# Performance work log

Measured on AMD Instinct MI355X. Metric: run time of the kernel, lower is better.

Reference implementation:

```python
import jax, jax.numpy as jnp
import numpy as np

N_NODES = 100000
HIDDEN = 128
N_EDGES = 1600000


def setup_inputs() -> dict:
    key = jax.random.key(0)
    k_x, k_w, k_r, k_c = jax.random.split(key, 4)
    x = jax.random.normal(k_x, (4, N_NODES, HIDDEN), dtype=jnp.float32)
    W = jax.random.normal(k_w, (HIDDEN, HIDDEN), dtype=jnp.float32) * 0.05
    b = jnp.zeros((HIDDEN,), dtype=jnp.float32)
    # COO edge list of the block-diagonal adjacency (scipy.sparse.block_diag in original)
    rows = jax.random.randint(k_r, (N_EDGES,), 0, N_NODES, dtype=jnp.int64)
    cols = jax.random.randint(k_c, (N_EDGES,), 0, N_NODES, dtype=jnp.int64)
    return {"x": x, "W": W, "b": b, "rows": rows, "cols": cols}


def reference(x, W, b, rows, cols):
    n_nodes = x.shape[1]
    beta = x[3, :, 0]   # [N]
    gamma = x[3, :, 1]  # [N]
    # linear + sigmoid on S/I/R channels: [3, N, H]
    sir = jax.nn.sigmoid(jnp.einsum('snh,oh->sno', x[:3], W) + b)
    S, I = sir[0], sir[1]
    # AI[r] += I[c] for each edge (r, c) of block-diagonal adjacency
    AI = jax.ops.segment_sum(I[cols], rows, num_segments=n_nodes)
    dS = -beta[:, None] * AI * S
    dI = -dS - gamma[:, None] * I
    dR = gamma[:, None] * I
    return jnp.stack((dS, dI, dR, jnp.zeros_like(dS)))
```

## Files before the change

### kernel.cpp

```cpp
#include <hip/hip_runtime.h>
#include <math.h>

#define HD 128
#define BM 128

typedef short bf16x8 __attribute__((ext_vector_type(8)));
typedef float f32x4 __attribute__((ext_vector_type(4)));
typedef unsigned short u16;

static __device__ __forceinline__ u16 f2bf(float f) {
  unsigned int u = __float_as_uint(f);
  u += 0x7FFF + ((u >> 16) & 1);
  return (u16)(u >> 16);
}
static __device__ __forceinline__ float bf2f(u16 s) {
  return __uint_as_float(((unsigned int)s) << 16);
}

__global__ void __launch_bounds__(256) zero_kernel(float4* __restrict__ p, long n4) {
  long i = (long)blockIdx.x * blockDim.x + threadIdx.x;
  long stride = (long)gridDim.x * blockDim.x;
  float4 z = make_float4(0.f, 0.f, 0.f, 0.f);
  for (; i < n4; i += stride) p[i] = z;
}

__global__ void __launch_bounds__(256) hist_rows(const int* __restrict__ rows,
                                                 int* __restrict__ cnt, int n_edges) {
  int i = blockIdx.x * 256 + threadIdx.x;
  int stride = gridDim.x * 256;
  for (; i < n_edges; i += stride) atomicAdd(&cnt[rows[i]], 1);
}

#define SCAN_E 2048
__global__ void __launch_bounds__(256) scan_block(const int* __restrict__ cnt,
                                                  int* __restrict__ off,
                                                  int* __restrict__ bsum, int n) {
  __shared__ int tsum[256];
  int tid = threadIdx.x;
  int base = blockIdx.x * SCAN_E + tid * 8;
  int vals[8];
  int s = 0;
#pragma unroll
  for (int k = 0; k < 8; ++k) {
    int idx = base + k;
    vals[k] = (idx < n) ? cnt[idx] : 0;
    s += vals[k];
  }
  tsum[tid] = s;
  __syncthreads();
  for (int o = 1; o < 256; o <<= 1) {
    int add = (tid >= o) ? tsum[tid - o] : 0;
    __syncthreads();
    tsum[tid] += add;
    __syncthreads();
  }
  int tbase = tsum[tid] - s;
  int run = 0;
#pragma unroll
  for (int k = 0; k < 8; ++k) {
    int idx = base + k;
    if (idx < n) off[idx] = tbase + run;
    run += vals[k];
  }
  if (tid == 255) bsum[blockIdx.x] = tsum[255];
}

__global__ void __launch_bounds__(256) scan_add(int* __restrict__ off,
                                                const int* __restrict__ bsum,
                                                int nb, int n, int n_edges) {
  __shared__ int sAdd;
  if (threadIdx.x == 0) {
    int acc = 0;
    for (int i = 0; i < (int)blockIdx.x; ++i) acc += bsum[i];
    sAdd = acc;
  }
  __syncthreads();
  int add = sAdd;
  int base = blockIdx.x * SCAN_E + threadIdx.x * 8;
#pragma unroll
  for (int k = 0; k < 8; ++k) {
    int idx = base + k;
    if (idx < n) off[idx] += add;
  }
  if (blockIdx.x == 0 && threadIdx.x == 0) off[n] = n_edges;
}

__global__ void __launch_bounds__(512, 4) fill_gemm(
    const float* __restrict__ x, const float* __restrict__ W,
    const float* __restrict__ b, float* __restrict__ SI, int nrows,
    const int* __restrict__ rows, const int* __restrict__ cols,
    const int* __restrict__ off, int* __restrict__ cursor,
    int* __restrict__ ecol, int n_edges, int fblocks) {
  __shared__ u16 Wh[HD * HD];
  __shared__ u16 Wl[HD * HD];

  int tid = threadIdx.x;
  if (blockIdx.x < fblocks) {
    int i = blockIdx.x * 512 + tid;
    int stride = fblocks * 512;
    for (; i < n_edges; i += stride) {
      int r = rows[i];
      int p = atomicAdd(&cursor[r], 1);
      ecol[off[r] + p] = cols[i];
    }
    return;
  }

  for (int idx = tid; idx < HD * (HD / 8); idx += 512) {
    int r = idx >> 4;
    int c = idx & 15;
    const float4* src = (const float4*)(W + r * HD + c * 8);
    float4 a0 = src[0], a1 = src[1];
    float f[8] = {a0.x, a0.y, a0.z, a0.w, a1.x, a1.y, a1.z, a1.w};
    union { u16 s[8]; uint4 v; } Ph, Pl;
#pragma unroll
    for (int i = 0; i < 8; ++i) {
      u16 h = f2bf(f[i]);
      Ph.s[i] = h;
      Pl.s[i] = f2bf(f[i] - bf2f(h));
    }
    int dst = r * HD + ((c ^ (r & 15)) << 3);
    *(uint4*)&Wh[dst] = Ph.v;
    *(uint4*)&Wl[dst] = Pl.v;
  }
  __syncthreads();

  int w = tid >> 6;
  int l = tid & 63;
  int lr = l & 15;
  int lk = l >> 4;
  int rbase = (blockIdx.x - fblocks) * BM + w * 16;
  int arow = rbase + lr;
  bool rowok = arow < nrows;

  bf16x8 ah[4], al[4];
#pragma unroll
  for (int s = 0; s < 4; ++s) {
    float f[8] = {0.f, 0.f, 0.f, 0.f, 0.f, 0.f, 0.f, 0.f};
    if (rowok) {
      const float4* src = (const float4*)(x + (long)arow * HD + (s * 4 + lk) * 8);
      float4 a0 = src[0], a1 = src[1];
      f[0] = a0.x; f[1] = a0.y; f[2] = a0.z; f[3] = a0.w;
      f[4] = a1.x; f[5] = a1.y; f[6] = a1.z; f[7] = a1.w;
    }
    union { u16 s16[8]; bf16x8 v; } Ph, Pl;
#pragma unroll
    for (int i = 0; i < 8; ++i) {
      u16 h = f2bf(f[i]);
      Ph.s16[i] = h;
      Pl.s16[i] = f2bf(f[i] - bf2f(h));
    }
    ah[s] = Ph.v;
    al[s] = Pl.v;
  }

#pragma unroll
  for (int ct = 0; ct < 8; ++ct) {
    int col = ct * 16 + lr;
    f32x4 acc = {0.f, 0.f, 0.f, 0.f};
#pragma unroll
    for (int s = 0; s < 4; ++s) {
      int cb = ((s * 4 + lk) ^ lr) << 3;
      bf16x8 bh = *(const bf16x8*)&Wh[col * HD + cb];
      bf16x8 bl = *(const bf16x8*)&Wl[col * HD + cb];
      acc = __builtin_amdgcn_mfma_f32_16x16x32_bf16(ah[s], bh, acc, 0, 0, 0);
      acc = __builtin_amdgcn_mfma_f32_16x16x32_bf16(al[s], bh, acc, 0, 0, 0);
      acc = __builtin_amdgcn_mfma_f32_16x16x32_bf16(ah[s], bl, acc, 0, 0, 0);
    }
    float bb = b[col];
#pragma unroll
    for (int j = 0; j < 4; ++j) {
      int grow = rbase + lk * 4 + j;
      if (grow < nrows) {
        float v = acc[j] + bb;
        SI[(long)grow * HD + col] = 1.f / (1.f + __expf(-v));
      }
    }
  }
}

__global__ void __launch_bounds__(256) gather_finalize(const float* __restrict__ S,
                                                       const float* __restrict__ I,
                                                       const float* __restrict__ x3,
                                                       const int* __restrict__ off,
                                                       const int* __restrict__ ecol,
                                                       float* __restrict__ out,
                                                       int n_nodes) {
  int node = blockIdx.x * 4 + (threadIdx.x >> 6);
  if (node >= n_nodes) return;
  int lane = threadIdx.x & 63;

  int beg = off[node], end = off[node + 1];
  float2 acc = make_float2(0.f, 0.f);
  for (int j0 = beg; j0 < end; j0 += 64) {
    int myc = (j0 + lane < end) ? ecol[j0 + lane] : 0;
    int cnt = min(64, end - j0);
    int j = 0;
    for (; j + 3 < cnt; j += 4) {
      int c0 = __shfl(myc, j);
      int c1 = __shfl(myc, j + 1);
      int c2 = __shfl(myc, j + 2);
      int c3 = __shfl(myc, j + 3);
      float2 v0 = ((const float2*)(I + (long)c0 * HD))[lane];
      float2 v1 = ((const float2*)(I + (long)c1 * HD))[lane];
      float2 v2 = ((const float2*)(I + (long)c2 * HD))[lane];
      float2 v3 = ((const float2*)(I + (long)c3 * HD))[lane];
      acc.x += (v0.x + v1.x) + (v2.x + v3.x);
      acc.y += (v0.y + v1.y) + (v2.y + v3.y);
    }
    for (; j < cnt; ++j) {
      int c0 = __shfl(myc, j);
      float2 v0 = ((const float2*)(I + (long)c0 * HD))[lane];
      acc.x += v0.x;
      acc.y += v0.y;
    }
  }

  float beta  = x3[(long)node * HD + 0];
  float gamma = x3[(long)node * HD + 1];
  float2 s  = ((const float2*)(S + (long)node * HD))[lane];
  float2 ii = ((const float2*)(I + (long)node * HD))[lane];

  float2 dS, dI, dR;
  dS.x = -beta * acc.x * s.x;
  dS.y = -beta * acc.y * s.y;
  dI.x = -dS.x - gamma * ii.x;
  dI.y = -dS.y - gamma * ii.y;
  dR.x = gamma * ii.x;
  dR.y = gamma * ii.y;

  long p = (long)node * (HD / 2) + lane;
  long plane = (long)n_nodes * (HD / 2);
  float2* o = (float2*)out;
  o[p] = dS;
  o[plane + p] = dI;
  o[2 * plane + p] = dR;
  o[3 * plane + p] = make_float2(0.f, 0.f);
}

extern "C" void kernel_launch(void* const* d_in, const int* in_sizes, int n_in,
                              void* d_out, int out_size, void* d_ws, size_t ws_size,
                              hipStream_t stream) {
  const float* x = (const float*)d_in[0];
  const float* W = (const float*)d_in[1];
  const float* b = (const float*)d_in[2];
  const int* rows = (const int*)d_in[3];
  const int* cols = (const int*)d_in[4];
  float* out = (float*)d_out;

  int n_nodes = in_sizes[0] / (4 * HD);
  int n_edges = in_sizes[3];
  int nrows = 2 * n_nodes;

  float* S = (float*)d_ws;
  float* I = S + (long)n_nodes * HD;
  int* ib = (int*)(I + (long)n_nodes * HD);
  int npad = (n_nodes + 11) & ~3;
  int* counts  = ib;
  int* cursor  = counts + npad;
  int* offsets = cursor + npad;
  int* bsum    = offsets + npad;
  int* ecol    = bsum + 256;

  zero_kernel<<<(2 * npad / 4 + 255) / 256, 256, 0, stream>>>(
      (float4*)counts, 2 * npad / 4);

  hist_rows<<<512, 256, 0, stream>>>(rows, counts, n_edges);

  int nb = (n_nodes + SCAN_E - 1) / SCAN_E;
  scan_block<<<nb, 256, 0, stream>>>(counts, offsets, bsum, n_nodes);
  scan_add<<<nb, 256, 0, stream>>>(offsets, bsum, nb, n_nodes, n_edges);

  int gblocks = (nrows + BM - 1) / BM;
  int fblocks = 192;
  fill_gemm<<<fblocks + gblocks, 512, 0, stream>>>(
      x, W, b, S, nrows, rows, cols, offsets, cursor, ecol, n_edges, fblocks);

  int gfb = (n_nodes + 3) / 4;
  gather_finalize<<<gfb, 256, 0, stream>>>(S, I, x + 3 * (long)n_nodes * HD,
                                           offsets, ecol, out, n_nodes);
}
```

Before: 602.4 us.

## Fuse CSR build and GEMM into one persistent cooperative kernel with grid syncs

```diff
diff --git a/kernel.cpp b/kernel.cpp
--- a/kernel.cpp
+++ b/kernel.cpp
@@ -1,8 +1,13 @@
 #include <hip/hip_runtime.h>
+#include <hip/hip_cooperative_groups.h>
 #include <math.h>
+
+namespace cg = cooperative_groups;
 
 #define HD 128
 #define BM 128
+#define SCAN_E 2048
+#define HIST_B 64
 
 typedef short bf16x8 __attribute__((ext_vector_type(8)));
 typedef float f32x4 __attribute__((ext_vector_type(4)));
@@ -17,165 +22,157 @@
   return __uint_as_float(((unsigned int)s) << 16);
 }
 
-__global__ void __launch_bounds__(256) zero_kernel(float4* __restrict__ p, long n4) {
-  long i = (long)blockIdx.x * blockDim.x + threadIdx.x;
-  long stride = (long)gridDim.x * blockDim.x;
-  float4 z = make_float4(0.f, 0.f, 0.f, 0.f);
-  for (; i < n4; i += stride) p[i] = z;
-}
-
-__global__ void __launch_bounds__(256) hist_rows(const int* __restrict__ rows,
-                                                 int* __restrict__ cnt, int n_edges) {
-  int i = blockIdx.x * 256 + threadIdx.x;
-  int stride = gridDim.x * 256;
-  for (; i < n_edges; i += stride) atomicAdd(&cnt[rows[i]], 1);
-}
-
-#define SCAN_E 2048
-__global__ void __launch_bounds__(256) scan_block(const int* __restrict__ cnt,
-                                                  int* __restrict__ off,
-                                                  int* __restrict__ bsum, int n) {
-  __shared__ int tsum[256];
-  int tid = threadIdx.x;
-  int base = blockIdx.x * SCAN_E + tid * 8;
-  int vals[8];
-  int s = 0;
-#pragma unroll
-  for (int k = 0; k < 8; ++k) {
-    int idx = base + k;
-    vals[k] = (idx < n) ? cnt[idx] : 0;
-    s += vals[k];
-  }
-  tsum[tid] = s;
-  __syncthreads();
-  for (int o = 1; o < 256; o <<= 1) {
-    int add = (tid >= o) ? tsum[tid - o] : 0;
-    __syncthreads();
-    tsum[tid] += add;
-    __syncthreads();
-  }
-  int tbase = tsum[tid] - s;
-  int run = 0;
-#pragma unroll
-  for (int k = 0; k < 8; ++k) {
-    int idx = base + k;
-    if (idx < n) off[idx] = tbase + run;
-    run += vals[k];
-  }
-  if (tid == 255) bsum[blockIdx.x] = tsum[255];
-}
-
-__global__ void __launch_bounds__(256) scan_add(int* __restrict__ off,
-                                                const int* __restrict__ bsum,
-                                                int nb, int n, int n_edges) {
-  __shared__ int sAdd;
-  if (threadIdx.x == 0) {
-    int acc = 0;
-    for (int i = 0; i < (int)blockIdx.x; ++i) acc += bsum[i];
-    sAdd = acc;
-  }
-  __syncthreads();
-  int add = sAdd;
-  int base = blockIdx.x * SCAN_E + threadIdx.x * 8;
-#pragma unroll
-  for (int k = 0; k < 8; ++k) {
-    int idx = base + k;
-    if (idx < n) off[idx] += add;
-  }
-  if (blockIdx.x == 0 && threadIdx.x == 0) off[n] = n_edges;
-}
-
-__global__ void __launch_bounds__(512, 4) fill_gemm(
+__global__ void __launch_bounds__(512, 4) build_gemm_coop(
     const float* __restrict__ x, const float* __restrict__ W,
     const float* __restrict__ b, float* __restrict__ SI, int nrows,
     const int* __restrict__ rows, const int* __restrict__ cols,
-    const int* __restrict__ off, int* __restrict__ cursor,
-    int* __restrict__ ecol, int n_edges, int fblocks) {
+    int* __restrict__ counts, int* __restrict__ cursor,
+    int* __restrict__ offsets, int* __restrict__ bsum,
+    int* __restrict__ ecol, int n_edges, int n_nodes, int ntiles) {
+  cg::grid_group grid = cg::this_grid();
   __shared__ u16 Wh[HD * HD];
   __shared__ u16 Wl[HD * HD];
 
   int tid = threadIdx.x;
-  if (blockIdx.x < fblocks) {
-    int i = blockIdx.x * 512 + tid;
-    int stride = fblocks * 512;
-    for (; i < n_edges; i += stride) {
-      int r = rows[i];
-      int p = atomicAdd(&cursor[r], 1);
-      ecol[off[r] + p] = cols[i];
-    }
-    return;
-  }
-
-  for (int idx = tid; idx < HD * (HD / 8); idx += 512) {
-    int r = idx >> 4;
-    int c = idx & 15;
-    const float4* src = (const float4*)(W + r * HD + c * 8);
-    float4 a0 = src[0], a1 = src[1];
-    float f[8] = {a0.x, a0.y, a0.z, a0.w, a1.x, a1.y, a1.z, a1.w};
-    union { u16 s[8]; uint4 v; } Ph, Pl;
-#pragma unroll
-    for (int i = 0; i < 8; ++i) {
-      u16 h = f2bf(f[i]);
-      Ph.s[i] = h;
-      Pl.s[i] = f2bf(f[i] - bf2f(h));
-    }
-    int dst = r * HD + ((c ^ (r & 15)) << 3);
-    *(uint4*)&Wh[dst] = Ph.v;
-    *(uint4*)&Wl[dst] = Pl.v;
-  }
-  __syncthreads();
-
-  int w = tid >> 6;
-  int l = tid & 63;
-  int lr = l & 15;
-  int lk = l >> 4;
-  int rbase = (blockIdx.x - fblocks) * BM + w * 16;
-  int arow = rbase + lr;
-  bool rowok = arow < nrows;
-
-  bf16x8 ah[4], al[4];
-#pragma unroll
-  for (int s = 0; s < 4; ++s) {
-    float f[8] = {0.f, 0.f, 0.f, 0.f, 0.f, 0.f, 0.f, 0.f};
-    if (rowok) {
-      const float4* src = (const float4*)(x + (long)arow * HD + (s * 4 + lk) * 8);
+  int bid = blockIdx.x;
+  int B = gridDim.x;
+
+  for (int i = bid * 512 + tid; i < n_nodes; i += B * 512) counts[i] = 0;
+  grid.sync();
+
+  if (bid < HIST_B) {
+    for (int i = bid * 512 + tid; i < n_edges; i += HIST_B * 512)
+      atomicAdd(&counts[rows[i]], 1);
+  } else {
+    for (int idx = tid; idx < HD * (HD / 8); idx += 512) {
+      int r = idx >> 4;
+      int c = idx & 15;
+      const float4* src = (const float4*)(W + r * HD + c * 8);
       float4 a0 = src[0], a1 = src[1];
-      f[0] = a0.x; f[1] = a0.y; f[2] = a0.z; f[3] = a0.w;
-      f[4] = a1.x; f[5] = a1.y; f[6] = a1.z; f[7] = a1.w;
-    }
-    union { u16 s16[8]; bf16x8 v; } Ph, Pl;
-#pragma unroll
-    for (int i = 0; i < 8; ++i) {
-      u16 h = f2bf(f[i]);
-      Ph.s16[i] = h;
-      Pl.s16[i] = f2bf(f[i] - bf2f(h));
-    }
-    ah[s] = Ph.v;
-    al[s] = Pl.v;
-  }
-
-#pragma unroll
-  for (int ct = 0; ct < 8; ++ct) {
-    int col = ct * 16 + lr;
-    f32x4 acc = {0.f, 0.f, 0.f, 0.f};
-#pragma unroll
-    for (int s = 0; s < 4; ++s) {
-      int cb = ((s * 4 + lk) ^ lr) << 3;
-      bf16x8 bh = *(const bf16x8*)&Wh[col * HD + cb];
-      bf16x8 bl = *(const bf16x8*)&Wl[col * HD + cb];
-      acc = __builtin_amdgcn_mfma_f32_16x16x32_bf16(ah[s], bh, acc, 0, 0, 0);
-      acc = __builtin_amdgcn_mfma_f32_16x16x32_bf16(al[s], bh, acc, 0, 0, 0);
-      acc = __builtin_amdgcn_mfma_f32_16x16x32_bf16(ah[s], bl, acc, 0, 0, 0);
-    }
-    float bb = b[col];
-#pragma unroll
-    for (int j = 0; j < 4; ++j) {
-      int grow = rbase + lk * 4 + j;
-      if (grow < nrows) {
-        float v = acc[j] + bb;
-        SI[(long)grow * HD + col] = 1.f / (1.f + __expf(-v));
-      }
-    }
+      float f[8] = {a0.x, a0.y, a0.z, a0.w, a1.x, a1.y, a1.z, a1.w};
+      union { u16 s[8]; uint4 v; } Ph, Pl;
+#pragma unroll
+      for (int i = 0; i < 8; ++i) {
+        u16 h = f2bf(f[i]);
+        Ph.s[i] = h;
+        Pl.s[i] = f2bf(f[i] - bf2f(h));
+      }
+      int dst = r * HD + ((c ^ (r & 15)) << 3);
+      *(uint4*)&Wh[dst] = Ph.v;
+      *(uint4*)&Wl[dst] = Pl.v;
+    }
+    __syncthreads();
+
+    int w = tid >> 6;
+    int l = tid & 63;
+    int lr = l & 15;
+    int lk = l >> 4;
+    for (int tile = bid - HIST_B; tile < ntiles; tile += B - HIST_B) {
+      int rbase = tile * BM + w * 16;
+      int arow = rbase + lr;
+      bool rowok = arow < nrows;
+
+      bf16x8 ah[4], al[4];
+#pragma unroll
+      for (int s = 0; s < 4; ++s) {
+        float f[8] = {0.f, 0.f, 0.f, 0.f, 0.f, 0.f, 0.f, 0.f};
+        if (rowok) {
+          const float4* src = (const float4*)(x + (long)arow * HD + (s * 4 + lk) * 8);
+          float4 a0 = src[0], a1 = src[1];
+          f[0] = a0.x; f[1] = a0.y; f[2] = a0.z; f[3] = a0.w;
+          f[4] = a1.x; f[5] = a1.y; f[6] = a1.z; f[7] = a1.w;
+        }
+        union { u16 s16[8]; bf16x8 v; } Ph, Pl;
+#pragma unroll
+        for (int i = 0; i < 8; ++i) {
+          u16 h = f2bf(f[i]);
+          Ph.s16[i] = h;
+          Pl.s16[i] = f2bf(f[i] - bf2f(h));
+        }
+        ah[s] = Ph.v;
+        al[s] = Pl.v;
+      }
+
+#pragma unroll
+      for (int ct = 0; ct < 8; ++ct) {
+        int col = ct * 16 + lr;
+        f32x4 acc = {0.f, 0.f, 0.f, 0.f};
+#pragma unroll
+        for (int s = 0; s < 4; ++s) {
+          int cb = ((s * 4 + lk) ^ lr) << 3;
+          bf16x8 bh = *(const bf16x8*)&Wh[col * HD + cb];
+          bf16x8 bl = *(const bf16x8*)&Wl[col * HD + cb];
+          acc = __builtin_amdgcn_mfma_f32_16x16x32_bf16(ah[s], bh, acc, 0, 0, 0);
+          acc = __builtin_amdgcn_mfma_f32_16x16x32_bf16(al[s], bh, acc, 0, 0, 0);
+          acc = __builtin_amdgcn_mfma_f32_16x16x32_bf16(ah[s], bl, acc, 0, 0, 0);
+        }
+        float bb = b[col];
+#pragma unroll
+        for (int j = 0; j < 4; ++j) {
+          int grow = rbase + lk * 4 + j;
+          if (grow < nrows) {
+            float v = acc[j] + bb;
+            SI[(long)grow * HD + col] = 1.f / (1.f + __expf(-v));
+          }
+        }
+      }
+    }
+  }
+  grid.sync();
+
+  int NB = (n_nodes + SCAN_E - 1) / SCAN_E;
+  int* tsum = (int*)Wh;
+  if (bid < NB) {
+    int base = bid * SCAN_E + tid * 4;
+    int vals[4];
+    int s = 0;
+#pragma unroll
+    for (int k = 0; k < 4; ++k) {
+      int idx = base + k;
+      vals[k] = (idx < n_nodes) ? counts[idx] : 0;
+      s += vals[k];
+    }
+    tsum[tid] = s;
+    __syncthreads();
+    for (int o = 1; o < 512; o <<= 1) {
+      int add = (tid >= o) ? tsum[tid - o] : 0;
+      __syncthreads();
+      tsum[tid] += add;
+      __syncthreads();
+    }
+    int tbase = tsum[tid] - s;
+    int run = 0;
+#pragma unroll
+    for (int k = 0; k < 4; ++k) {
+      int idx = base + k;
+      if (idx < n_nodes) offsets[idx] = tbase + run;
+      run += vals[k];
+    }
+    if (tid == 511) bsum[bid] = tsum[511];
+  }
+  grid.sync();
+
+  if (bid < NB) {
+    int add = 0;
+    for (int i = 0; i < bid; ++i) add += bsum[i];
+    int base = bid * SCAN_E + tid * 4;
+#pragma unroll
+    for (int k = 0; k < 4; ++k) {
+      int idx = base + k;
+      if (idx < n_nodes) {
+        int o2 = offsets[idx] + add;
+        offsets[idx] = o2;
+        cursor[idx] = o2;
+      }
+    }
+    if (bid == 0 && tid == 0) offsets[n_nodes] = n_edges;
+  }
+  grid.sync();
+
+  for (int i = bid * 512 + tid; i < n_edges; i += B * 512) {
+    int r = rows[i];
+    int p = atomicAdd(&cursor[r], 1);
+    ecol[p] = cols[i];
   }
 }
 
@@ -251,6 +248,7 @@
   int n_nodes = in_sizes[0] / (4 * HD);
   int n_edges = in_sizes[3];
   int nrows = 2 * n_nodes;
+  int ntiles = (nrows + BM - 1) / BM;
 
   float* S = (float*)d_ws;
   float* I = S + (long)n_nodes * HD;
@@ -262,19 +260,22 @@
   int* bsum    = offsets + npad;
   int* ecol    = bsum + 256;
 
-  zero_kernel<<<(2 * npad / 4 + 255) / 256, 256, 0, stream>>>(
-      (float4*)counts, 2 * npad / 4);
-
-  hist_rows<<<512, 256, 0, stream>>>(rows, counts, n_edges);
-
-  int nb = (n_nodes + SCAN_E - 1) / SCAN_E;
-  scan_block<<<nb, 256, 0, stream>>>(counts, offsets, bsum, n_nodes);
-  scan_add<<<nb, 256, 0, stream>>>(offsets, bsum, nb, n_nodes, n_edges);
-
-  int gblocks = (nrows + BM - 1) / BM;
-  int fblocks = 192;
-  fill_gemm<<<fblocks + gblocks, 512, 0, stream>>>(
-      x, W, b, S, nrows, rows, cols, offsets, cursor, ecol, n_edges, fblocks);
+  static int coopGrid = 0;
+  if (coopGrid == 0) {
+    int perCU = 0;
+    hipError_t e = hipOccupancyMaxActiveBlocksPerMultiprocessor(
+        &perCU, build_gemm_coop, 512, 0);
+    if (e != hipSuccess || perCU < 1) perCU = 1;
+    if (perCU > 4) perCU = 4;
+    coopGrid = perCU * 256;
+  }
+
+  void* args[] = {(void*)&x, (void*)&W, (void*)&b, (void*)&S, (void*)&nrows,
+                  (void*)&rows, (void*)&cols, (void*)&counts, (void*)&cursor,
+                  (void*)&offsets, (void*)&bsum, (void*)&ecol,
+                  (void*)&n_edges, (void*)&n_nodes, (void*)&ntiles};
+  hipLaunchCooperativeKernel((const void*)build_gemm_coop, dim3(coopGrid),
+                             dim3(512), args, 0, stream);
 
   int gfb = (n_nodes + 3) / 4;
   gather_finalize<<<gfb, 256, 0, stream>>>(S, I, x + 3 * (long)n_nodes * HD,
```

New measurement: 961.1 us. 59.5% more time.
